# Kernel tuning notes

Hardware: AMD Instinct MI355X
Metric: run time of the kernel (lower is better)

## Reference

```python
import jax, jax.numpy as jnp
import numpy as np

N = 100000      # nodes
E = 640000      # edges
VOCAB = 100     # Embedding(num_embeddings=100)
EMB = 10        # embed_dim
H = 128         # GCN hidden width


def gcn_conv(x, W, b, src, dst, n):
    """PyG GCNConv: linear (no bias) -> add self loops -> sym-normalized scatter-add -> +bias."""
    x = x @ W                                  # [n, out]
    loop = jnp.arange(n, dtype=src.dtype)
    src2 = jnp.concatenate([src, loop])        # [E+n]
    dst2 = jnp.concatenate([dst, loop])
    deg = jax.ops.segment_sum(jnp.ones_like(dst2, dtype=x.dtype), dst2, num_segments=n)
    dinv = jnp.where(deg > 0, jax.lax.rsqrt(deg), 0.0)
    norm = dinv[src2] * dinv[dst2]             # [E+n]
    out = jax.ops.segment_sum(x[src2] * norm[:, None], dst2, num_segments=n)
    return out + b


def setup_inputs() -> dict:
    key = jax.random.key(0)
    ks = jax.random.split(key, 9)
    x = jax.random.randint(ks[0], (N, 1), 0, VOCAB, dtype=jnp.int32)
    edge_index = jax.random.randint(ks[1], (2, E), 0, N, dtype=jnp.int32)
    batch = jnp.zeros((N,), dtype=jnp.int32)
    emb = jax.random.normal(ks[2], (VOCAB, EMB), dtype=jnp.float32)
    W1 = jax.random.normal(ks[3], (EMB, H), dtype=jnp.float32) * 0.1
    b1 = jnp.zeros((H,), dtype=jnp.float32)
    W2 = jax.random.normal(ks[4], (H, H), dtype=jnp.float32) * 0.1
    b2 = jnp.zeros((H,), dtype=jnp.float32)
    W3 = jax.random.normal(ks[5], (H, 1), dtype=jnp.float32) * 0.1
    b3 = jnp.zeros((1,), dtype=jnp.float32)
    return {"x": x, "edge_index": edge_index, "batch": batch,
            "emb": emb, "W1": W1, "b1": b1, "W2": W2, "b2": b2, "W3": W3, "b3": b3}


def reference(x, edge_index, batch, emb, W1, b1, W2, b2, W3, b3):
    # eval mode: dropout(p=0.5) is identity
    h = emb[x[:, 0]]                           # [N, EMB] embedding lookup + squeeze
    src, dst = edge_index[0], edge_index[1]
    n = h.shape[0]
    h = jax.nn.relu(gcn_conv(h, W1, b1, src, dst, n))   # [N, 128]
    h = jax.nn.relu(gcn_conv(h, W2, b2, src, dst, n))   # [N, 128]
    out = jax.nn.sigmoid((h @ W3 + b3).reshape(-1))      # [N]
    return out
```

## Files before the change

kernel.cpp:

```cpp
#include <hip/hip_runtime.h>
#include <math.h>

#define HDIM 128
#define EMBD 10
#define CAP  64
#define ZSTRIDE 136

typedef __attribute__((ext_vector_type(8))) short short8;
typedef __attribute__((ext_vector_type(8))) unsigned short ushort8;
typedef __attribute__((ext_vector_type(4))) float float4a;

__device__ inline ushort bf16_rne(float f) {
    unsigned u = __float_as_uint(f);
    unsigned r = (u + 0x7fffu + ((u >> 16) & 1u)) >> 16;
    return (ushort)r;
}
__device__ inline float bf16_to_f(ushort u) {
    return __uint_as_float(((unsigned)u) << 16);
}

__global__ void k_prep(const float* __restrict__ emb, const float* __restrict__ W1,
                       const float* __restrict__ W2, ushort* __restrict__ Tb,
                       ushort* __restrict__ W2t, int* __restrict__ cnt,
                       int N, int vocab) {
    int t = blockIdx.x * 256 + threadIdx.x;
    if (t < N) cnt[t] = 0;
    if (t < vocab * HDIM) {
        int c = t >> 7, f = t & 127;
        float s = 0.f;
#pragma unroll
        for (int k = 0; k < EMBD; ++k) s += emb[c * EMBD + k] * W1[k * HDIM + f];
        Tb[t] = bf16_rne(s);
    }
    if (t < HDIM * HDIM) {
        int n = t >> 7, k = t & 127;
        W2t[t] = bf16_rne(W2[k * HDIM + n]);
    }
}

__global__ void k_fill(const int* __restrict__ src, const int* __restrict__ dst,
                       int* __restrict__ cnt, int* __restrict__ slot, int E) {
    int e = blockIdx.x * blockDim.x + threadIdx.x;
    if (e >= E) return;
    int d = dst[e];
    int p = atomicAdd(&cnt[d], 1);
    if (p < CAP) slot[(size_t)d * CAP + p] = src[e];
}

__global__ __launch_bounds__(256) void k_gather1(const int* __restrict__ slot,
                                                 const int* __restrict__ cnt,
                                                 const int* __restrict__ x,
                                                 const ushort* __restrict__ Tb,
                                                 const float* __restrict__ b1,
                                                 ushort* __restrict__ A, int N) {
    int tid = blockIdx.x * 256 + threadIdx.x;
    int v = tid >> 4, q = tid & 15;
    if (v >= N) return;
    int deg = cnt[v];
    int m = min(deg, CAP);
    float dv = rsqrtf((float)deg + 1.0f);

    int cq = x[v]; float wq = 0.f;
    if (q < m) {
        int s = slot[(size_t)v * CAP + q];
        cq = x[s];
        wq = rsqrtf((float)cnt[s] + 1.0f);
    } else if (q == m) {
        wq = dv;
    }
    int   cs[16]; float ws[16];
#pragma unroll
    for (int t = 0; t < 16; ++t) {
        cs[t] = __shfl(cq, t, 16);
        ws[t] = __shfl(wq, t, 16);
    }
    ushort8 rows[16];
#pragma unroll
    for (int t = 0; t < 16; ++t)
        rows[t] = *(const ushort8*)(Tb + (size_t)cs[t] * HDIM + q * 8);
    float acc[8] = {0.f, 0.f, 0.f, 0.f, 0.f, 0.f, 0.f, 0.f};
#pragma unroll
    for (int t = 0; t < 16; ++t) {
#pragma unroll
        for (int k = 0; k < 8; ++k) acc[k] += ws[t] * bf16_to_f(rows[t][k]);
    }
    for (int base = 16; base < m; base += 16) {
        int j = base + q;
        int cj = x[v]; float wj = 0.f;
        if (j < m) {
            int s = slot[(size_t)v * CAP + j];
            cj = x[s];
            wj = rsqrtf((float)cnt[s] + 1.0f);
        }
#pragma unroll
        for (int t = 0; t < 16; ++t) {
            int c = __shfl(cj, t, 16);
            float ww = __shfl(wj, t, 16);
            ushort8 y = *(const ushort8*)(Tb + (size_t)c * HDIM + q * 8);
#pragma unroll
            for (int k = 0; k < 8; ++k) acc[k] += ww * bf16_to_f(y[k]);
        }
    }
    if (m >= 16) {
        ushort8 y = *(const ushort8*)(Tb + (size_t)x[v] * HDIM + q * 8);
#pragma unroll
        for (int k = 0; k < 8; ++k) acc[k] += dv * bf16_to_f(y[k]);
    }
    float4 bb0 = *(const float4*)(b1 + q * 8);
    float4 bb1 = *(const float4*)(b1 + q * 8 + 4);
    float bb[8] = {bb0.x, bb0.y, bb0.z, bb0.w, bb1.x, bb1.y, bb1.z, bb1.w};
    ushort8 o;
#pragma unroll
    for (int k = 0; k < 8; ++k)
        o[k] = bf16_rne(fmaxf(dv * acc[k] + bb[k], 0.f));
    *(ushort8*)(A + (size_t)v * HDIM + q * 8) = o;
}

__global__ __launch_bounds__(256) void k_conv2(const int* __restrict__ slot,
                                               const int* __restrict__ cnt,
                                               const ushort* __restrict__ A,
                                               const ushort* __restrict__ W2t,
                                               const float* __restrict__ b2,
                                               const float* __restrict__ W3,
                                               const float* __restrict__ b3,
                                               float* __restrict__ out, int N) {
    __shared__ ushort Z[16 * ZSTRIDE];
    __shared__ float pbuf[4][16];
    int tid = threadIdx.x;
    int g = tid >> 4, q = tid & 15;
    int v0 = blockIdx.x * 16;
    int v = min(v0 + g, N - 1);

    int deg = cnt[v];
    int m = min(deg, CAP);
    float dv = rsqrtf((float)deg + 1.0f);

    int sq = v; float wq = 0.f;
    if (q < m) {
        sq = slot[(size_t)v * CAP + q];
        wq = rsqrtf((float)cnt[sq] + 1.0f);
    } else if (q == m) {
        wq = dv;
    }
    int   ss[16]; float ws[16];
#pragma unroll
    for (int t = 0; t < 16; ++t) {
        ss[t] = __shfl(sq, t, 16);
        ws[t] = __shfl(wq, t, 16);
    }
    ushort8 rows[16];
#pragma unroll
    for (int t = 0; t < 16; ++t)
        rows[t] = *(const ushort8*)(A + (size_t)ss[t] * HDIM + q * 8);
    float acc[8] = {0.f, 0.f, 0.f, 0.f, 0.f, 0.f, 0.f, 0.f};
#pragma unroll
    for (int t = 0; t < 16; ++t) {
#pragma unroll
        for (int k = 0; k < 8; ++k) acc[k] += ws[t] * bf16_to_f(rows[t][k]);
    }
    for (int base = 16; base < m; base += 16) {
        int j = base + q;
        int sj = v; float wj = 0.f;
        if (j < m) {
            sj = slot[(size_t)v * CAP + j];
            wj = rsqrtf((float)cnt[sj] + 1.0f);
        }
#pragma unroll
        for (int t = 0; t < 16; ++t) {
            int s = __shfl(sj, t, 16);
            float ww = __shfl(wj, t, 16);
            ushort8 y = *(const ushort8*)(A + (size_t)s * HDIM + q * 8);
#pragma unroll
            for (int k = 0; k < 8; ++k) acc[k] += ww * bf16_to_f(y[k]);
        }
    }
    if (m >= 16) {
        ushort8 y = *(const ushort8*)(A + (size_t)v * HDIM + q * 8);
#pragma unroll
        for (int k = 0; k < 8; ++k) acc[k] += dv * bf16_to_f(y[k]);
    }
    ushort8 z;
#pragma unroll
    for (int k = 0; k < 8; ++k) z[k] = bf16_rne(dv * acc[k]);
    *(ushort8*)&Z[g * ZSTRIDE + q * 8] = z;
    __syncthreads();

    int lane = tid & 63, w = tid >> 6;
    int l15 = lane & 15, g4 = lane >> 4;
    short8 af[4];
#pragma unroll
    for (int kt = 0; kt < 4; ++kt)
        af[kt] = *(const short8*)&Z[l15 * ZSTRIDE + kt * 32 + g4 * 8];

    float pr[4] = {0.f, 0.f, 0.f, 0.f};
#pragma unroll
    for (int i = 0; i < 2; ++i) {
        int nt = w * 2 + i;
        int col = nt * 16 + l15;
        const ushort* bp = W2t + (size_t)col * HDIM + g4 * 8;
        float4a accD = {0.f, 0.f, 0.f, 0.f};
#pragma unroll
        for (int kt = 0; kt < 4; ++kt) {
            short8 bf = *(const short8*)(bp + kt * 32);
            accD = __builtin_amdgcn_mfma_f32_16x16x32_bf16(af[kt], bf, accD, 0, 0, 0);
        }
        float bc = b2[col], wc = W3[col];
#pragma unroll
        for (int r = 0; r < 4; ++r)
            pr[r] += fmaxf(accD[r] + bc, 0.f) * wc;
    }
#pragma unroll
    for (int off = 1; off < 16; off <<= 1) {
#pragma unroll
        for (int r = 0; r < 4; ++r) pr[r] += __shfl_xor(pr[r], off, 16);
    }
    if (l15 == 0) {
#pragma unroll
        for (int r = 0; r < 4; ++r) pbuf[w][g4 * 4 + r] = pr[r];
    }
    __syncthreads();
    if (tid < 16) {
        int row = tid;
        float s = pbuf[0][row] + pbuf[1][row] + pbuf[2][row] + pbuf[3][row];
        int vr = v0 + row;
        if (vr < N) out[vr] = 1.f / (1.f + expf(-(s + b3[0])));
    }
}

extern "C" void kernel_launch(void* const* d_in, const int* in_sizes, int n_in,
                              void* d_out, int out_size, void* d_ws, size_t ws_size,
                              hipStream_t stream) {
    const int*   x    = (const int*)d_in[0];
    const int*   ei   = (const int*)d_in[1];
    const float* emb  = (const float*)d_in[3];
    const float* W1   = (const float*)d_in[4];
    const float* b1   = (const float*)d_in[5];
    const float* W2   = (const float*)d_in[6];
    const float* b2   = (const float*)d_in[7];
    const float* W3   = (const float*)d_in[8];
    const float* b3   = (const float*)d_in[9];
    float*       out  = (float*)d_out;

    int N = in_sizes[0];
    int E = in_sizes[1] / 2;
    int vocab = in_sizes[3] / EMBD;
    const int* src = ei;
    const int* dst = ei + E;

    char* w = (char*)d_ws;
    ushort* Tb   = (ushort*)w;  w += (size_t)vocab * HDIM * 2;
    ushort* A    = (ushort*)w;  w += (size_t)N * HDIM * 2;
    ushort* W2t  = (ushort*)w;  w += (size_t)HDIM * HDIM * 2;
    int*    cnt  = (int*)w;     w += (size_t)N * 4;
    int*    slot = (int*)w;     w += (size_t)N * CAP * 4;

    int prep_elems = N;
    if (vocab * HDIM > prep_elems) prep_elems = vocab * HDIM;
    if (HDIM * HDIM > prep_elems) prep_elems = HDIM * HDIM;
    k_prep<<<(prep_elems + 255) / 256, 256, 0, stream>>>(emb, W1, W2, Tb, W2t, cnt, N, vocab);
    k_fill<<<(E + 255) / 256, 256, 0, stream>>>(src, dst, cnt, slot, E);

    int gblocks = (int)(((long long)N * 16 + 255) / 256);
    k_gather1<<<gblocks, 256, 0, stream>>>(slot, cnt, x, Tb, b1, A, N);

    int cblocks = (N + 15) / 16;
    k_conv2<<<cblocks, 256, 0, stream>>>(slot, cnt, A, W2t, b2, W3, b3, out, N);
}
```

Before: 184.0 us.

## Prescale layer-1 output by source norm, pack node metadata, stage embedding table in LDS

Layer 1 now writes its activations already multiplied by the source-side normalisation factor. Layer 2 can then sum neighbour rows with unit weights, with no per-edge rsqrt or cnt lookup. A new k_meta kernel packs each node's class id and bf16 degree-norm into one word, so the layer-1 gather does a single dependent load per neighbour. The 100x128 bf16 projected embedding table is copied into shared memory per 512-thread block. The costs are an extra kernel launch, a per-block LDS fill of about 25KB, bf16 rounding of the norm weights, and a hardcoded vocab of 100 in the shared-memory array size.

```diff
diff --git a/kernel.cpp b/kernel.cpp
--- a/kernel.cpp
+++ b/kernel.cpp
@@ -47,62 +47,64 @@
     if (p < CAP) slot[(size_t)d * CAP + p] = src[e];
 }
 
-__global__ __launch_bounds__(256) void k_gather1(const int* __restrict__ slot,
+__global__ void k_meta(const int* __restrict__ x, const int* __restrict__ cnt,
+                       unsigned* __restrict__ meta, int N) {
+    int v = blockIdx.x * 256 + threadIdx.x;
+    if (v >= N) return;
+    meta[v] = ((unsigned)x[v] << 16) | (unsigned)bf16_rne(rsqrtf((float)cnt[v] + 1.0f));
+}
+
+__global__ __launch_bounds__(512) void k_gather1(const int* __restrict__ slot,
                                                  const int* __restrict__ cnt,
-                                                 const int* __restrict__ x,
+                                                 const unsigned* __restrict__ meta,
                                                  const ushort* __restrict__ Tb,
                                                  const float* __restrict__ b1,
-                                                 ushort* __restrict__ A, int N) {
-    int tid = blockIdx.x * 256 + threadIdx.x;
+                                                 ushort* __restrict__ Ap,
+                                                 int N, int vocab) {
+    __shared__ ushort TbL[100 * HDIM];
+    int n8 = (vocab * HDIM) >> 3;
+    for (int i = threadIdx.x; i < n8; i += 512)
+        ((ushort8*)TbL)[i] = ((const ushort8*)Tb)[i];
+    __syncthreads();
+
+    int tid = blockIdx.x * 512 + threadIdx.x;
     int v = tid >> 4, q = tid & 15;
     if (v >= N) return;
     int deg = cnt[v];
     int m = min(deg, CAP);
     float dv = rsqrtf((float)deg + 1.0f);
 
-    int cq = x[v]; float wq = 0.f;
-    if (q < m) {
-        int s = slot[(size_t)v * CAP + q];
-        cq = x[s];
-        wq = rsqrtf((float)cnt[s] + 1.0f);
-    } else if (q == m) {
-        wq = dv;
-    }
-    int   cs[16]; float ws[16];
+    unsigned mv = meta[(q < m) ? slot[(size_t)v * CAP + q] : v];
+    int cq = mv >> 16;
+    float wq = (q < m) ? bf16_to_f((ushort)(mv & 0xffffu))
+                       : ((q == m) ? dv : 0.f);
+
+    float acc[8] = {0.f, 0.f, 0.f, 0.f, 0.f, 0.f, 0.f, 0.f};
 #pragma unroll
     for (int t = 0; t < 16; ++t) {
-        cs[t] = __shfl(cq, t, 16);
-        ws[t] = __shfl(wq, t, 16);
-    }
-    ushort8 rows[16];
-#pragma unroll
-    for (int t = 0; t < 16; ++t)
-        rows[t] = *(const ushort8*)(Tb + (size_t)cs[t] * HDIM + q * 8);
-    float acc[8] = {0.f, 0.f, 0.f, 0.f, 0.f, 0.f, 0.f, 0.f};
-#pragma unroll
-    for (int t = 0; t < 16; ++t) {
-#pragma unroll
-        for (int k = 0; k < 8; ++k) acc[k] += ws[t] * bf16_to_f(rows[t][k]);
+        int c = __shfl(cq, t, 16);
+        float ww = __shfl(wq, t, 16);
+        ushort8 y = *(const ushort8*)&TbL[c * HDIM + q * 8];
+#pragma unroll
+        for (int k = 0; k < 8; ++k) acc[k] += ww * bf16_to_f(y[k]);
     }
     for (int base = 16; base < m; base += 16) {
         int j = base + q;
-        int cj = x[v]; float wj = 0.f;
-        if (j < m) {
-            int s = slot[(size_t)v * CAP + j];
-            cj = x[s];
-            wj = rsqrtf((float)cnt[s] + 1.0f);
-        }
+        unsigned mj = meta[(j < m) ? slot[(size_t)v * CAP + j] : v];
+        int cj = mj >> 16;
+        float wj = (j < m) ? bf16_to_f((ushort)(mj & 0xffffu)) : 0.f;
 #pragma unroll
         for (int t = 0; t < 16; ++t) {
             int c = __shfl(cj, t, 16);
             float ww = __shfl(wj, t, 16);
-            ushort8 y = *(const ushort8*)(Tb + (size_t)c * HDIM + q * 8);
+            ushort8 y = *(const ushort8*)&TbL[c * HDIM + q * 8];
 #pragma unroll
             for (int k = 0; k < 8; ++k) acc[k] += ww * bf16_to_f(y[k]);
         }
     }
     if (m >= 16) {
-        ushort8 y = *(const ushort8*)(Tb + (size_t)x[v] * HDIM + q * 8);
+        int c = meta[v] >> 16;
+        ushort8 y = *(const ushort8*)&TbL[c * HDIM + q * 8];
 #pragma unroll
         for (int k = 0; k < 8; ++k) acc[k] += dv * bf16_to_f(y[k]);
     }
@@ -112,18 +114,18 @@
     ushort8 o;
 #pragma unroll
     for (int k = 0; k < 8; ++k)
-        o[k] = bf16_rne(fmaxf(dv * acc[k] + bb[k], 0.f));
-    *(ushort8*)(A + (size_t)v * HDIM + q * 8) = o;
-}
-
-__global__ __launch_bounds__(256) void k_conv2(const int* __restrict__ slot,
-                                               const int* __restrict__ cnt,
-                                               const ushort* __restrict__ A,
-                                               const ushort* __restrict__ W2t,
-                                               const float* __restrict__ b2,
-                                               const float* __restrict__ W3,
-                                               const float* __restrict__ b3,
-                                               float* __restrict__ out, int N) {
+        o[k] = bf16_rne(dv * fmaxf(dv * acc[k] + bb[k], 0.f));
+    *(ushort8*)(Ap + (size_t)v * HDIM + q * 8) = o;
+}
+
+__global__ __launch_bounds__(256, 4) void k_conv2(const int* __restrict__ slot,
+                                                  const int* __restrict__ cnt,
+                                                  const ushort* __restrict__ Ap,
+                                                  const ushort* __restrict__ W2t,
+                                                  const float* __restrict__ b2,
+                                                  const float* __restrict__ W3,
+                                                  const float* __restrict__ b3,
+                                                  float* __restrict__ out, int N) {
     __shared__ ushort Z[16 * ZSTRIDE];
     __shared__ float pbuf[4][16];
     int tid = threadIdx.x;
@@ -135,49 +137,37 @@
     int m = min(deg, CAP);
     float dv = rsqrtf((float)deg + 1.0f);
 
-    int sq = v; float wq = 0.f;
-    if (q < m) {
-        sq = slot[(size_t)v * CAP + q];
-        wq = rsqrtf((float)cnt[sq] + 1.0f);
-    } else if (q == m) {
-        wq = dv;
-    }
-    int   ss[16]; float ws[16];
+    int sq = (q < m) ? slot[(size_t)v * CAP + q] : v;
+
+    ushort8 rows[16];
 #pragma unroll
     for (int t = 0; t < 16; ++t) {
-        ss[t] = __shfl(sq, t, 16);
-        ws[t] = __shfl(wq, t, 16);
-    }
-    ushort8 rows[16];
-#pragma unroll
-    for (int t = 0; t < 16; ++t)
-        rows[t] = *(const ushort8*)(A + (size_t)ss[t] * HDIM + q * 8);
+        int s = __shfl(sq, t, 16);
+        rows[t] = *(const ushort8*)(Ap + (size_t)s * HDIM + q * 8);
+    }
     float acc[8] = {0.f, 0.f, 0.f, 0.f, 0.f, 0.f, 0.f, 0.f};
 #pragma unroll
     for (int t = 0; t < 16; ++t) {
-#pragma unroll
-        for (int k = 0; k < 8; ++k) acc[k] += ws[t] * bf16_to_f(rows[t][k]);
+        float wt = (t <= m) ? 1.f : 0.f;
+#pragma unroll
+        for (int k = 0; k < 8; ++k) acc[k] += wt * bf16_to_f(rows[t][k]);
     }
     for (int base = 16; base < m; base += 16) {
         int j = base + q;
-        int sj = v; float wj = 0.f;
-        if (j < m) {
-            sj = slot[(size_t)v * CAP + j];
-            wj = rsqrtf((float)cnt[sj] + 1.0f);
-        }
+        int sj = (j < m) ? slot[(size_t)v * CAP + j] : v;
 #pragma unroll
         for (int t = 0; t < 16; ++t) {
             int s = __shfl(sj, t, 16);
-            float ww = __shfl(wj, t, 16);
-            ushort8 y = *(const ushort8*)(A + (size_t)s * HDIM + q * 8);
-#pragma unroll
-            for (int k = 0; k < 8; ++k) acc[k] += ww * bf16_to_f(y[k]);
+            float wt = (base + t < m) ? 1.f : 0.f;
+            ushort8 y = *(const ushort8*)(Ap + (size_t)s * HDIM + q * 8);
+#pragma unroll
+            for (int k = 0; k < 8; ++k) acc[k] += wt * bf16_to_f(y[k]);
         }
     }
     if (m >= 16) {
-        ushort8 y = *(const ushort8*)(A + (size_t)v * HDIM + q * 8);
-#pragma unroll
-        for (int k = 0; k < 8; ++k) acc[k] += dv * bf16_to_f(y[k]);
+        ushort8 y = *(const ushort8*)(Ap + (size_t)v * HDIM + q * 8);
+#pragma unroll
+        for (int k = 0; k < 8; ++k) acc[k] += bf16_to_f(y[k]);
     }
     ushort8 z;
 #pragma unroll
@@ -248,21 +238,23 @@
     const int* dst = ei + E;
 
     char* w = (char*)d_ws;
-    ushort* Tb   = (ushort*)w;  w += (size_t)vocab * HDIM * 2;
-    ushort* A    = (ushort*)w;  w += (size_t)N * HDIM * 2;
-    ushort* W2t  = (ushort*)w;  w += (size_t)HDIM * HDIM * 2;
-    int*    cnt  = (int*)w;     w += (size_t)N * 4;
-    int*    slot = (int*)w;     w += (size_t)N * CAP * 4;
+    ushort*   Tb   = (ushort*)w;    w += (size_t)vocab * HDIM * 2;
+    ushort*   Ap   = (ushort*)w;    w += (size_t)N * HDIM * 2;
+    ushort*   W2t  = (ushort*)w;    w += (size_t)HDIM * HDIM * 2;
+    int*      cnt  = (int*)w;       w += (size_t)N * 4;
+    unsigned* meta = (unsigned*)w;  w += (size_t)N * 4;
+    int*      slot = (int*)w;       w += (size_t)N * CAP * 4;
 
     int prep_elems = N;
     if (vocab * HDIM > prep_elems) prep_elems = vocab * HDIM;
     if (HDIM * HDIM > prep_elems) prep_elems = HDIM * HDIM;
     k_prep<<<(prep_elems + 255) / 256, 256, 0, stream>>>(emb, W1, W2, Tb, W2t, cnt, N, vocab);
     k_fill<<<(E + 255) / 256, 256, 0, stream>>>(src, dst, cnt, slot, E);
-
-    int gblocks = (int)(((long long)N * 16 + 255) / 256);
-    k_gather1<<<gblocks, 256, 0, stream>>>(slot, cnt, x, Tb, b1, A, N);
+    k_meta<<<(N + 255) / 256, 256, 0, stream>>>(x, cnt, meta, N);
+
+    int g1blocks = (int)(((long long)N * 16 + 511) / 512);
+    k_gather1<<<g1blocks, 512, 0, stream>>>(slot, cnt, meta, Tb, b1, Ap, N, vocab);
 
     int cblocks = (N + 15) / 16;
-    k_conv2<<<cblocks, 256, 0, stream>>>(slot, cnt, A, W2t, b2, W3, b3, out, N);
-}
+    k_conv2<<<cblocks, 256, 0, stream>>>(slot, cnt, Ap, W2t, b2, W3, b3, out, N);
+}
```

New measurement: 179.9 us. 1.02x faster.
